# Kernel tuning notes

Measured on AMD Instinct MI355X. Metric: run time of the kernel, lower is better.

## Reference

```python
import jax, jax.numpy as jnp
import numpy as np

VOCAB = 100000
DIM = 300
SEQ = 200
BATCH = 1024


def setup_inputs() -> dict:
    key = jax.random.key(0)
    ks = jax.random.split(key, 7)
    tokens = jax.random.randint(ks[0], (SEQ, BATCH), 0, VOCAB, dtype=jnp.int32)
    static_lut = jax.random.normal(ks[1], (VOCAB, DIM), dtype=jnp.float32)
    # lut = pretrained vectors + N(0, 0.01) noise
    lut = static_lut + 0.01 * jax.random.normal(ks[2], (VOCAB, DIM), dtype=jnp.float32)
    W1 = jax.random.normal(ks[3], (600, 600), dtype=jnp.float32) / np.sqrt(600.0)
    b1 = jnp.zeros((600,), dtype=jnp.float32)
    W2 = jax.random.normal(ks[4], (1, 600), dtype=jnp.float32) / np.sqrt(600.0)
    b2 = jnp.zeros((1,), dtype=jnp.float32)
    return {"tokens": tokens, "lut": lut, "static_lut": static_lut,
            "W1": W1, "b1": b1, "W2": W2, "b2": b2}


def _first_occurrence_mask(tokens):
    # tokens: [S, B]. mask[i, b] = 1 iff tokens[i, b] is the first occurrence
    # of that token value in column b (emulates per-column set() dedup).
    S = tokens.shape[0]
    eq = tokens[:, None, :] == tokens[None, :, :]          # [S, S, B]
    first_idx = jnp.argmax(eq, axis=1)                      # [S, B] first j with same token
    return (first_idx == jnp.arange(S, dtype=first_idx.dtype)[:, None])


def reference(tokens, lut, static_lut, W1, b1, W2, b2):
    mask = _first_occurrence_mask(tokens).astype(lut.dtype)  # [S, B]
    # dedup embedding-bag sums over unique tokens per column
    e_learn = jnp.einsum('sbd,sb->bd', lut[tokens], mask)          # [B, 300]
    e_static = jnp.einsum('sbd,sb->bd', static_lut[tokens], mask)  # [B, 300]
    hidden = jnp.concatenate([e_learn, e_static], axis=-1)         # [B, 600]
    h = jax.nn.relu(hidden @ W1.T + b1)                            # [B, 600]
    out = h @ W2.T + b2                                            # [B, 1]
    return out[:, 0]                                               # [B]
```

## Files before the change

### kernel.cpp

```cpp
#include <hip/hip_runtime.h>

#define SEQ   200
#define BATCH 1024
#define DIM   300
#define HID   600
#define VOCAB 100000

#define NQ     4
#define SCHUNK (SEQ / NQ)

#define BW    4
#define JCH   12
#define JPER  (HID / JCH)

#define HIDDEN_ELEMS (BATCH * HID)
#define HIDDEN_BYTES ((size_t)HIDDEN_ELEMS * 4)

__global__ __launch_bounds__(192) void embed_part_kernel(
    const int* __restrict__ tokens,
    const float* __restrict__ lut,
    const float* __restrict__ slut,
    float* __restrict__ hid4) {
  const int b   = blockIdx.x;
  const int q   = blockIdx.y;
  const int tid = threadIdx.x;

  __shared__ int   toks[SEQ];
  __shared__ float keep[SCHUNK];

  for (int s = tid; s < SEQ; s += 192) toks[s] = tokens[s * BATCH + b];
  __syncthreads();

  const int s0 = q * SCHUNK;
  if (tid < SCHUNK) {
    const int s = s0 + tid;
    const int t = toks[s];
    float m = 1.f;
    for (int p = 0; p < s; ++p) {
      if (toks[p] == t) { m = 0.f; break; }
    }
    keep[tid] = m;
  }
  __syncthreads();

  const int tab_i = tid / 75;
  const int slot  = tid % 75;
  if (tab_i < 2) {
    const float* __restrict__ tab = tab_i ? slut : lut;
    float4 a = make_float4(0.f, 0.f, 0.f, 0.f);
#pragma unroll 5
    for (int i = 0; i < SCHUNK; ++i) {
      const float  m = keep[i];
      const float4 v = ((const float4*)(tab + (size_t)toks[s0 + i] * DIM))[slot];
      a.x += m * v.x; a.y += m * v.y; a.z += m * v.z; a.w += m * v.w;
    }
    float* dst = hid4 + ((size_t)q * BATCH + b) * HID + tab_i * DIM;
    ((float4*)dst)[slot] = a;
  }
}

__global__ __launch_bounds__(256) void combine_kernel(
    const float* __restrict__ hid4, float* __restrict__ hidden) {
  const int i = blockIdx.x * 256 + threadIdx.x;
  const int n4 = HIDDEN_ELEMS / 4;
  if (i < n4) {
    const float4* p = (const float4*)hid4;
    const float4 a = p[i];
    const float4 b = p[i + n4];
    const float4 c = p[i + 2 * n4];
    const float4 d = p[i + 3 * n4];
    float4 s;
    s.x = (a.x + b.x) + (c.x + d.x);
    s.y = (a.y + b.y) + (c.y + d.y);
    s.z = (a.z + b.z) + (c.z + d.z);
    s.w = (a.w + b.w) + (c.w + d.w);
    ((float4*)hidden)[i] = s;
  }
}

__global__ __launch_bounds__(256) void out_init_kernel(
    float* __restrict__ out, const float* __restrict__ b2) {
  const int i = blockIdx.x * 256 + threadIdx.x;
  if (i < BATCH) out[i] = b2[0];
}

template <int CTRL>
__device__ __forceinline__ float dpp_add(float x) {
  const int y = __builtin_amdgcn_update_dpp(
      0, __float_as_int(x), CTRL, 0xf, 0xf, true);
  return x + __int_as_float(y);
}

__device__ __forceinline__ float wave_sum(float h) {
  h = dpp_add<0x111>(h);
  h = dpp_add<0x112>(h);
  h = dpp_add<0x114>(h);
  h = dpp_add<0x118>(h);
  h = dpp_add<0x142>(h);
  h = dpp_add<0x143>(h);
  return h;
}

__global__ __launch_bounds__(256) void mlp_kernel(
    const float* __restrict__ hidden,
    const float* __restrict__ W1,
    const float* __restrict__ b1,
    const float* __restrict__ W2,
    float* __restrict__ out) {
  const int wave = threadIdx.x >> 6;
  const int lane = threadIdx.x & 63;
  const int b0   = (blockIdx.x * 4 + wave) * BW;
  const int j0   = blockIdx.y * JPER;

  float a[BW][10];
#pragma unroll
  for (int bb = 0; bb < BW; ++bb) {
    const float* __restrict__ hb = hidden + (size_t)(b0 + bb) * HID;
#pragma unroll
    for (int i = 0; i < 9; ++i) a[bb][i] = hb[lane + 64 * i];
    a[bb][9] = (lane < 24) ? hb[lane + 576] : 0.f;
  }

  float acc[BW] = {0.f, 0.f, 0.f, 0.f};

#pragma unroll 2
  for (int jj = 0; jj < JPER; ++jj) {
    const int j = j0 + jj;
    const float* __restrict__ wr = W1 + (size_t)j * HID;
    float d0 = 0.f, d1 = 0.f, d2 = 0.f, d3 = 0.f;
#pragma unroll
    for (int i = 0; i < 9; ++i) {
      const float w = wr[lane + 64 * i];
      d0 += a[0][i] * w;
      d1 += a[1][i] * w;
      d2 += a[2][i] * w;
      d3 += a[3][i] * w;
    }
    {
      const float w = (lane < 24) ? wr[lane + 576] : 0.f;
      d0 += a[0][9] * w;
      d1 += a[1][9] * w;
      d2 += a[2][9] * w;
      d3 += a[3][9] * w;
    }
    d0 = wave_sum(d0); d1 = wave_sum(d1);
    d2 = wave_sum(d2); d3 = wave_sum(d3);
    const float b1j = b1[j];
    const float w2j = W2[j];
    acc[0] += fmaxf(d0 + b1j, 0.f) * w2j;
    acc[1] += fmaxf(d1 + b1j, 0.f) * w2j;
    acc[2] += fmaxf(d2 + b1j, 0.f) * w2j;
    acc[3] += fmaxf(d3 + b1j, 0.f) * w2j;
  }

  if (lane == 63) {
#pragma unroll
    for (int bb = 0; bb < BW; ++bb) atomicAdd(&out[b0 + bb], acc[bb]);
  }
}

extern "C" void kernel_launch(void* const* d_in, const int* in_sizes, int n_in,
                              void* d_out, int out_size, void* d_ws, size_t ws_size,
                              hipStream_t stream) {
  const int*   tokens = (const int*)  d_in[0];
  const float* lut    = (const float*)d_in[1];
  const float* slut   = (const float*)d_in[2];
  const float* W1     = (const float*)d_in[3];
  const float* b1     = (const float*)d_in[4];
  const float* W2     = (const float*)d_in[5];
  const float* b2     = (const float*)d_in[6];
  float* out = (float*)d_out;

  float* hid4   = (float*)d_ws;
  float* hidden = (float*)((char*)d_ws + (size_t)NQ * HIDDEN_BYTES);

  out_init_kernel<<<(BATCH + 255) / 256, 256, 0, stream>>>(out, b2);
  embed_part_kernel<<<dim3(BATCH, NQ), 192, 0, stream>>>(
      tokens, lut, slut, hid4);
  combine_kernel<<<(HIDDEN_ELEMS / 4 + 255) / 256, 256, 0, stream>>>(
      hid4, hidden);
  mlp_kernel<<<dim3(BATCH / (4 * BW), JCH), 256, 0, stream>>>(
      hidden, W1, b1, W2, out);
}
```

Baseline: 130.6 us.

## Split embedding gather into two vocab-range passes and skip masked rows

The embedding gather now runs as two launches, each covering half the vocabulary range, with each block taking half the sequence instead of a quarter. The idea is to shrink the table footprint each pass touches so more of it stays in cache. Rows that are duplicates or outside the current range are skipped with a branch rather than multiplied by zero, which avoids useless loads. The cost is reading the tokens twice, running the dedup scan twice, and divergent branches across the wave.

```diff
diff --git a/kernel.cpp b/kernel.cpp
--- a/kernel.cpp
+++ b/kernel.cpp
@@ -6,8 +6,9 @@
 #define HID   600
 #define VOCAB 100000
 
-#define NQ     4
-#define SCHUNK (SEQ / NQ)
+#define NSCH   2
+#define SCH    (SEQ / NSCH)
+#define RSPLIT 50000
 
 #define BW    4
 #define JCH   12
@@ -20,19 +21,20 @@
     const int* __restrict__ tokens,
     const float* __restrict__ lut,
     const float* __restrict__ slut,
-    float* __restrict__ hid4) {
+    float* __restrict__ hid4,
+    int lo, int hi, int qbase) {
   const int b   = blockIdx.x;
-  const int q   = blockIdx.y;
+  const int sc  = blockIdx.y;
   const int tid = threadIdx.x;
 
   __shared__ int   toks[SEQ];
-  __shared__ float keep[SCHUNK];
+  __shared__ float keep[SCH];
 
   for (int s = tid; s < SEQ; s += 192) toks[s] = tokens[s * BATCH + b];
   __syncthreads();
 
-  const int s0 = q * SCHUNK;
-  if (tid < SCHUNK) {
+  const int s0 = sc * SCH;
+  if (tid < SCH) {
     const int s = s0 + tid;
     const int t = toks[s];
     float m = 1.f;
@@ -48,13 +50,14 @@
   if (tab_i < 2) {
     const float* __restrict__ tab = tab_i ? slut : lut;
     float4 a = make_float4(0.f, 0.f, 0.f, 0.f);
-#pragma unroll 5
-    for (int i = 0; i < SCHUNK; ++i) {
-      const float  m = keep[i];
-      const float4 v = ((const float4*)(tab + (size_t)toks[s0 + i] * DIM))[slot];
-      a.x += m * v.x; a.y += m * v.y; a.z += m * v.z; a.w += m * v.w;
+    for (int i = 0; i < SCH; ++i) {
+      const int t = toks[s0 + i];
+      if ((keep[i] != 0.f) & (t >= lo) & (t < hi)) {
+        const float4 v = ((const float4*)(tab + (size_t)t * DIM))[slot];
+        a.x += v.x; a.y += v.y; a.z += v.z; a.w += v.w;
+      }
     }
-    float* dst = hid4 + ((size_t)q * BATCH + b) * HID + tab_i * DIM;
+    float* dst = hid4 + ((size_t)(qbase + sc) * BATCH + b) * HID + tab_i * DIM;
     ((float4*)dst)[slot] = a;
   }
 }
@@ -172,11 +175,13 @@
   float* out = (float*)d_out;
 
   float* hid4   = (float*)d_ws;
-  float* hidden = (float*)((char*)d_ws + (size_t)NQ * HIDDEN_BYTES);
+  float* hidden = (float*)((char*)d_ws + 4 * HIDDEN_BYTES);
 
   out_init_kernel<<<(BATCH + 255) / 256, 256, 0, stream>>>(out, b2);
-  embed_part_kernel<<<dim3(BATCH, NQ), 192, 0, stream>>>(
-      tokens, lut, slut, hid4);
+  embed_part_kernel<<<dim3(BATCH, NSCH), 192, 0, stream>>>(
+      tokens, lut, slut, hid4, 0, RSPLIT, 0);
+  embed_part_kernel<<<dim3(BATCH, NSCH), 192, 0, stream>>>(
+      tokens, lut, slut, hid4, RSPLIT, VOCAB, 2);
   combine_kernel<<<(HIDDEN_ELEMS / 4 + 255) / 256, 256, 0, stream>>>(
       hid4, hidden);
   mlp_kernel<<<dim3(BATCH / (4 * BW), JCH), 256, 0, stream>>>(
```

Result: slower. 150.9 us (+15.6%).

## Compact and sort unique tokens per column before gathering embedding rows

Applied to the files above, without the earlier changes.

Each block now runs the dedup check over the whole column, writes the unique tokens (padded with INT_MAX) into shared memory and bitonic-sorts them, then splits only the unique tokens across the four partial-sum blocks. This drops the masked multiply and skips gathers for duplicate tokens, and the sorted order may improve DRAM locality. The cost is that every one of the four blocks per column repeats the full O(S^2) dedup and a 36-step bitonic sort with a barrier after each step. With random tokens over a 100k vocabulary, duplicates are rare, so few gathers are actually skipped.

```diff
diff --git a/kernel.cpp b/kernel.cpp
--- a/kernel.cpp
+++ b/kernel.cpp
@@ -1,4 +1,5 @@
 #include <hip/hip_runtime.h>
+#include <limits.h>
 
 #define SEQ   200
 #define BATCH 1024
@@ -6,8 +7,7 @@
 #define HID   600
 #define VOCAB 100000
 
-#define NQ     4
-#define SCHUNK (SEQ / NQ)
+#define NQ    4
 
 #define BW    4
 #define JCH   12
@@ -16,7 +16,7 @@
 #define HIDDEN_ELEMS (BATCH * HID)
 #define HIDDEN_BYTES ((size_t)HIDDEN_ELEMS * 4)
 
-__global__ __launch_bounds__(192) void embed_part_kernel(
+__global__ __launch_bounds__(256) void embed_sort_kernel(
     const int* __restrict__ tokens,
     const float* __restrict__ lut,
     const float* __restrict__ slut,
@@ -25,34 +25,53 @@
   const int q   = blockIdx.y;
   const int tid = threadIdx.x;
 
-  __shared__ int   toks[SEQ];
-  __shared__ float keep[SCHUNK];
-
-  for (int s = tid; s < SEQ; s += 192) toks[s] = tokens[s * BATCH + b];
+  __shared__ int toks[SEQ];
+  __shared__ int stok[256];
+  __shared__ int nk_sh;
+
+  for (int s = tid; s < SEQ; s += 256) toks[s] = tokens[s * BATCH + b];
+  if (tid == 0) nk_sh = 0;
   __syncthreads();
 
-  const int s0 = q * SCHUNK;
-  if (tid < SCHUNK) {
-    const int s = s0 + tid;
-    const int t = toks[s];
-    float m = 1.f;
-    for (int p = 0; p < s; ++p) {
-      if (toks[p] == t) { m = 0.f; break; }
-    }
-    keep[tid] = m;
-  }
+  int my = INT_MAX;
+  if (tid < SEQ) {
+    const int t = toks[tid];
+    bool k = true;
+    for (int p = 0; p < tid; ++p) {
+      if (toks[p] == t) { k = false; break; }
+    }
+    if (k) my = t;
+  }
+  stok[tid] = my;
+  if (my != INT_MAX) atomicAdd(&nk_sh, 1);
   __syncthreads();
+
+  for (int k = 2; k <= 256; k <<= 1) {
+    for (int j = k >> 1; j > 0; j >>= 1) {
+      const int ixj = tid ^ j;
+      if (ixj > tid) {
+        const int a = stok[tid];
+        const int c = stok[ixj];
+        const bool up = ((tid & k) == 0);
+        if ((a > c) == up) { stok[tid] = c; stok[ixj] = a; }
+      }
+      __syncthreads();
+    }
+  }
+
+  const int nk = nk_sh;
+  const int i0 = (q * nk) / NQ;
+  const int i1 = ((q + 1) * nk) / NQ;
 
   const int tab_i = tid / 75;
   const int slot  = tid % 75;
   if (tab_i < 2) {
     const float* __restrict__ tab = tab_i ? slut : lut;
     float4 a = make_float4(0.f, 0.f, 0.f, 0.f);
-#pragma unroll 5
-    for (int i = 0; i < SCHUNK; ++i) {
-      const float  m = keep[i];
-      const float4 v = ((const float4*)(tab + (size_t)toks[s0 + i] * DIM))[slot];
-      a.x += m * v.x; a.y += m * v.y; a.z += m * v.z; a.w += m * v.w;
+#pragma unroll 4
+    for (int i = i0; i < i1; ++i) {
+      const float4 v = ((const float4*)(tab + (size_t)stok[i] * DIM))[slot];
+      a.x += v.x; a.y += v.y; a.z += v.z; a.w += v.w;
     }
     float* dst = hid4 + ((size_t)q * BATCH + b) * HID + tab_i * DIM;
     ((float4*)dst)[slot] = a;
@@ -172,10 +191,10 @@
   float* out = (float*)d_out;
 
   float* hid4   = (float*)d_ws;
-  float* hidden = (float*)((char*)d_ws + (size_t)NQ * HIDDEN_BYTES);
+  float* hidden = (float*)((char*)d_ws + 4 * HIDDEN_BYTES);
 
   out_init_kernel<<<(BATCH + 255) / 256, 256, 0, stream>>>(out, b2);
-  embed_part_kernel<<<dim3(BATCH, NQ), 192, 0, stream>>>(
+  embed_sort_kernel<<<dim3(BATCH, NQ), 256, 0, stream>>>(
       tokens, lut, slut, hid4);
   combine_kernel<<<(HIDDEN_ELEMS / 4 + 255) / 256, 256, 0, stream>>>(
       hid4, hidden);
```

Result: no change. 129.0 us (-1.3%).
